# Kernel optimization log

Hardware: AMD Instinct MI355X
Metric: run time of the kernel (lower is better)

The kernel has to match this reference:

```python
import jax, jax.numpy as jnp
import numpy as np

N_NODES = 100000
EPS = 1e-12  # F.normalize eps


def _sage_conv(x, src, dst, deg, Wl, bl, Wr):
    # mean aggregation of neighbor (source) features at destination nodes
    agg = jax.ops.segment_sum(x[src], dst, num_segments=N_NODES)  # [N, F]
    agg = agg / jnp.maximum(deg, 1.0)[:, None]
    out = agg @ Wl + bl + x @ Wr  # lin_l(mean(x_j)) + lin_r(x_i)
    # normalize=True -> L2 row normalization
    norm = jnp.sqrt(jnp.sum(out * out, axis=-1, keepdims=True))
    return out / jnp.maximum(norm, EPS)


def setup_inputs() -> dict:
    key = jax.random.key(0)
    ks = jax.random.split(key, 10)
    F_IN, H, C = 14, 32, 2
    x = jax.random.normal(ks[0], (N_NODES, F_IN), dtype=jnp.float32)
    edge_index = jax.random.randint(ks[1], (2, 6400000), 0, N_NODES, dtype=jnp.int32)
    def glorot(k, shape):
        lim = float(np.sqrt(6.0 / (shape[0] + shape[1])))
        return jax.random.uniform(k, shape, jnp.float32, -lim, lim)
    return {
        "x": x,
        "edge_index": edge_index,
        "W1l": glorot(ks[2], (F_IN, H)), "b1": jnp.zeros((H,), jnp.float32),
        "W1r": glorot(ks[3], (F_IN, H)),
        "W2l": glorot(ks[4], (H, H)), "b2": jnp.zeros((H,), jnp.float32),
        "W2r": glorot(ks[5], (H, H)),
        "Wlin": glorot(ks[6], (H, C)), "blin": jnp.zeros((C,), jnp.float32),
    }


def reference(x, edge_index, W1l, b1, W1r, W2l, b2, W2r, Wlin, blin):
    src, dst = edge_index[0], edge_index[1]
    deg = jax.ops.segment_sum(jnp.ones_like(dst, dtype=x.dtype), dst,
                              num_segments=N_NODES)  # in-degree per node
    h = jax.nn.relu(_sage_conv(x, src, dst, deg, W1l, b1, W1r))
    # dropout p=0.2 is identity at inference
    h = jax.nn.relu(_sage_conv(h, src, dst, deg, W2l, b2, W2r))
    return h @ Wlin + blin  # [N, num_classes]
```

## Files before the change

kernel.cpp:

```cpp
#include <hip/hip_runtime.h>
#include <hip/hip_bf16.h>


#define CHA 16384
#define MAXBH 800
#define CAPH 9728

static __device__ __forceinline__ unsigned short f2bf(float f) {
    unsigned u = __float_as_uint(f);
    unsigned r = (u + 0x7FFFu + ((u >> 16) & 1u)) >> 16;
    return (unsigned short)r;
}
#define BF_LO(u) __uint_as_float((u) << 16)
#define BF_HI(u) __uint_as_float((u) & 0xFFFF0000u)

__global__ __launch_bounds__(1024) void partitionA(
        const float* __restrict__ x, unsigned short* __restrict__ xb,
        const int* __restrict__ src, const int* __restrict__ dst,
        int* __restrict__ bcursor, unsigned* __restrict__ part,
        int E, int N, int NBH) {
    __shared__ unsigned pk[CHA];
    __shared__ int h[MAXBH], lofs[MAXBH], delta[MAXBH];
    int t = threadIdx.x;
    int base = blockIdx.x * CHA;
    int end = base + CHA; if (end > E) end = E;
    int cnt = end - base;

    for (int i = blockIdx.x * 1024 + t; i < N * 16; i += gridDim.x * 1024) {
        int n = i >> 4, f = i & 15;
        float v = (f < 14) ? x[n * 14 + f] : 0.f;
        xb[i] = f2bf(v);
    }

    int ed[16], es[16], er[16];
    for (int i = t; i < NBH; i += 1024) h[i] = 0;
    __syncthreads();
    #pragma unroll
    for (int i = 0; i < 4; ++i) {
        int j = i * 4096 + t * 4;
        if (j + 4 <= cnt) {
            int4 d4 = *(const int4*)(dst + base + j);
            int4 s4 = *(const int4*)(src + base + j);
            ed[i*4+0] = d4.x; ed[i*4+1] = d4.y; ed[i*4+2] = d4.z; ed[i*4+3] = d4.w;
            es[i*4+0] = s4.x; es[i*4+1] = s4.y; es[i*4+2] = s4.z; es[i*4+3] = s4.w;
            er[i*4+0] = atomicAdd(&h[d4.x >> 7], 1);
            er[i*4+1] = atomicAdd(&h[d4.y >> 7], 1);
            er[i*4+2] = atomicAdd(&h[d4.z >> 7], 1);
            er[i*4+3] = atomicAdd(&h[d4.w >> 7], 1);
        } else {
            #pragma unroll
            for (int k = 0; k < 4; ++k) {
                if (j + k < cnt) {
                    ed[i*4+k] = dst[base + j + k];
                    es[i*4+k] = src[base + j + k];
                    er[i*4+k] = atomicAdd(&h[ed[i*4+k] >> 7], 1);
                } else ed[i*4+k] = -1;
            }
        }
    }
    __syncthreads();
    if (t < 64) {
        int vals[13];
        int run = 0;
        int b13 = t * 13;
        #pragma unroll
        for (int i = 0; i < 13; ++i) {
            int idx = b13 + i;
            int xv = (idx < NBH) ? h[idx] : 0;
            run += xv;
            vals[i] = run;
        }
        int tot = run, sc = run;
        #pragma unroll
        for (int off = 1; off < 64; off <<= 1) {
            int nv = __shfl_up(sc, off);
            if (t >= off) sc += nv;
        }
        int excl = sc - tot;
        #pragma unroll
        for (int i = 0; i < 13; ++i) {
            int idx = b13 + i;
            if (idx < NBH) {
                h[idx] = excl + vals[i];
                lofs[idx] = excl + (i ? vals[i - 1] : 0);
            }
        }
    }
    __syncthreads();
    if (t < NBH) {
        int excl = lofs[t];
        int v = h[t] - excl;
        int g = v ? atomicAdd(&bcursor[t], v) : 0;
        delta[t] = t * CAPH + g - excl;
    }
    __syncthreads();
    #pragma unroll
    for (int i = 0; i < 16; ++i) {
        int d = ed[i];
        if (d >= 0) {
            int b = d >> 7;
            pk[lofs[b] + er[i]] = ((unsigned)(d & 127) << 24) | (unsigned)es[i];
        }
    }
    __syncthreads();
    int wid = t >> 6, lane = t & 63;
    for (int b = wid; b < NBH; b += 16) {
        int s = lofs[b];
        int e2 = h[b];
        int dlt = delta[b];
        int lim = (b + 1) * CAPH;
        for (int k = s + lane; k < e2; k += 64) {
            int gidx = dlt + k;
            if (gidx < lim) part[gidx] = pk[k];
        }
    }
}

__global__ __launch_bounds__(1024) void partitionB_sort(
        const unsigned* __restrict__ part, const int* __restrict__ bcursor,
        int* __restrict__ deg, int* __restrict__ offs, int* __restrict__ nlo,
        int* __restrict__ sorted_src, int N, int HALF) {
    __shared__ int pk2[CAPH];
    __shared__ int hh[256], keyofs[256];
    __shared__ int sTot;
    int hbid = blockIdx.x;
    int t = threadIdx.x;
    int start = hbid * CAPH;
    int cc = bcursor[hbid];
    if (cc > CAPH) cc = CAPH;
    int end = start + cc;
    unsigned ce[10];
    int rk[10];
    if (t < 256) hh[t] = 0;
    __syncthreads();
    #pragma unroll
    for (int i = 0; i < 10; ++i) {
        int idx = start + t + i * 1024;
        unsigned p = 0xFFFFFFFFu;
        int r = 0;
        if (idx < end) {
            p = part[idx];
            int key = (int)(p >> 24) * 2 + (((int)(p & 0xFFFFFFu) < HALF) ? 0 : 1);
            r = atomicAdd(&hh[key], 1);
        }
        ce[i] = p;
        rk[i] = r;
    }
    __syncthreads();
    if (t < 64) {
        int b4 = t * 4;
        int v0 = hh[b4], v1 = hh[b4 + 1], v2 = hh[b4 + 2], v3 = hh[b4 + 3];
        int s1 = v0 + v1, s2 = s1 + v2, s3 = s2 + v3;
        int sc = s3;
        #pragma unroll
        for (int off = 1; off < 64; off <<= 1) {
            int nv = __shfl_up(sc, off);
            if (t >= off) sc += nv;
        }
        int excl = sc - s3;
        keyofs[b4]     = excl;
        keyofs[b4 + 1] = excl + v0;
        keyofs[b4 + 2] = excl + s1;
        keyofs[b4 + 3] = excl + s2;
        if (t == 63) sTot = excl + s3;
    }
    __syncthreads();
    if (t < 128) {
        int lo = hh[2 * t];
        int d = lo + hh[2 * t + 1];
        int excl = keyofs[2 * t];
        int node = hbid * 128 + t;
        if (node < N) {
            deg[node] = d;
            offs[node] = start + excl;
            nlo[node] = lo;
        }
    }
    #pragma unroll
    for (int i = 0; i < 10; ++i) {
        unsigned p = ce[i];
        if (p != 0xFFFFFFFFu) {
            int s = (int)(p & 0xFFFFFFu);
            int key = (int)(p >> 24) * 2 + ((s < HALF) ? 0 : 1);
            int pos = keyofs[key] + rk[i];
            if (pos < CAPH) pk2[pos] = s;
        }
    }
    __syncthreads();
    int tot = sTot; if (tot > CAPH) tot = CAPH;
    for (int i = t; i < tot; i += 1024)
        sorted_src[start + i] = pk2[i];
}

__global__ __launch_bounds__(256) void gather14_dense1(
        const uint4* __restrict__ xb4, const float* __restrict__ x,
        const int* __restrict__ sorted_src, const int* __restrict__ offs,
        const int* __restrict__ deg,
        const float* __restrict__ W1l, const float* __restrict__ b1,
        const float* __restrict__ W1r,
        float* __restrict__ hbuf, unsigned short* __restrict__ hb, int N) {
    __shared__ float swl[448], swr[448], sb1[32];
    int t = threadIdx.x;
    for (int i = t; i < 448; i += 256) { swl[i] = W1l[i]; swr[i] = W1r[i]; }
    if (t < 32) sb1[t] = b1[t];
    __syncthreads();

    int node = blockIdx.x * 32 + (t >> 3);
    int sub = t & 7, ep = sub >> 1, half = sub & 1;
    int lanebase = (t & 63) & ~7;
    bool valid = node < N;
    int js = valid ? offs[node] : 0;
    int d  = valid ? deg[node] : 0;
    int je = js + d;
    float x0 = 0.f, x1 = 0.f;
    if (valid && sub < 7) {
        x0 = x[node * 14 + sub * 2];
        x1 = x[node * 14 + sub * 2 + 1];
    }

    float a[8] = {0,0,0,0,0,0,0,0};
    int j = js + ep;
    for (; j + 12 < je; j += 16) {
        int s0 = sorted_src[j], s1 = sorted_src[j + 4];
        int s2 = sorted_src[j + 8], s3 = sorted_src[j + 12];
        uint4 u0 = xb4[s0 * 2 + half], u1 = xb4[s1 * 2 + half];
        uint4 u2 = xb4[s2 * 2 + half], u3 = xb4[s3 * 2 + half];
        a[0] += (BF_LO(u0.x) + BF_LO(u1.x)) + (BF_LO(u2.x) + BF_LO(u3.x));
        a[1] += (BF_HI(u0.x) + BF_HI(u1.x)) + (BF_HI(u2.x) + BF_HI(u3.x));
        a[2] += (BF_LO(u0.y) + BF_LO(u1.y)) + (BF_LO(u2.y) + BF_LO(u3.y));
        a[3] += (BF_HI(u0.y) + BF_HI(u1.y)) + (BF_HI(u2.y) + BF_HI(u3.y));
        a[4] += (BF_LO(u0.z) + BF_LO(u1.z)) + (BF_LO(u2.z) + BF_LO(u3.z));
        a[5] += (BF_HI(u0.z) + BF_HI(u1.z)) + (BF_HI(u2.z) + BF_HI(u3.z));
        a[6] += (BF_LO(u0.w) + BF_LO(u1.w)) + (BF_LO(u2.w) + BF_LO(u3.w));
        a[7] += (BF_HI(u0.w) + BF_HI(u1.w)) + (BF_HI(u2.w) + BF_HI(u3.w));
    }
    for (; j + 4 < je; j += 8) {
        int s0 = sorted_src[j], s1 = sorted_src[j + 4];
        uint4 u0 = xb4[s0 * 2 + half], u1 = xb4[s1 * 2 + half];
        a[0] += BF_LO(u0.x) + BF_LO(u1.x);
        a[1] += BF_HI(u0.x) + BF_HI(u1.x);
        a[2] += BF_LO(u0.y) + BF_LO(u1.y);
        a[3] += BF_HI(u0.y) + BF_HI(u1.y);
        a[4] += BF_LO(u0.z) + BF_LO(u1.z);
        a[5] += BF_HI(u0.z) + BF_HI(u1.z);
        a[6] += BF_LO(u0.w) + BF_LO(u1.w);
        a[7] += BF_HI(u0.w) + BF_HI(u1.w);
    }
    for (; j < je; j += 4) {
        uint4 u0 = xb4[sorted_src[j] * 2 + half];
        a[0] += BF_LO(u0.x); a[1] += BF_HI(u0.x);
        a[2] += BF_LO(u0.y); a[3] += BF_HI(u0.y);
        a[4] += BF_LO(u0.z); a[5] += BF_HI(u0.z);
        a[6] += BF_LO(u0.w); a[7] += BF_HI(u0.w);
    }
    #pragma unroll
    for (int i = 0; i < 8; ++i) {
        a[i] += __shfl_xor(a[i], 2);
        a[i] += __shfl_xor(a[i], 4);
    }

    float inv = 1.0f / ((d > 0) ? (float)d : 1.0f);
    float acc[4];
    #pragma unroll
    for (int i = 0; i < 4; ++i) acc[i] = sb1[sub * 4 + i];
    #pragma unroll
    for (int k = 0; k < 14; ++k) {
        float ag = __shfl(a[k & 7], lanebase + (k >> 3)) * inv;
        float xv = __shfl((k & 1) ? x1 : x0, lanebase + (k >> 1));
        float4 wl = *(const float4*)&swl[k * 32 + sub * 4];
        float4 wr = *(const float4*)&swr[k * 32 + sub * 4];
        acc[0] += ag * wl.x + xv * wr.x;
        acc[1] += ag * wl.y + xv * wr.y;
        acc[2] += ag * wl.z + xv * wr.z;
        acc[3] += ag * wl.w + xv * wr.w;
    }
    float ss = 0.f;
    #pragma unroll
    for (int i = 0; i < 4; ++i) ss += acc[i] * acc[i];
    ss += __shfl_xor(ss, 1); ss += __shfl_xor(ss, 2); ss += __shfl_xor(ss, 4);
    float invn = 1.f / fmaxf(sqrtf(ss), 1e-12f);
    if (valid) {
        float hv[4];
        #pragma unroll
        for (int i = 0; i < 4; ++i) hv[i] = fmaxf(acc[i] * invn, 0.f);
        *(float4*)(hbuf + (size_t)node * 32 + sub * 4) =
            make_float4(hv[0], hv[1], hv[2], hv[3]);
        uint2 pb;
        pb.x = (unsigned)f2bf(hv[0]) | ((unsigned)f2bf(hv[1]) << 16);
        pb.y = (unsigned)f2bf(hv[2]) | ((unsigned)f2bf(hv[3]) << 16);
        *(uint2*)(hb + (size_t)node * 32 + sub * 4) = pb;
    }
}

__global__ __launch_bounds__(256) void gather32_p0(
        const uint4* __restrict__ hb, const int* __restrict__ sorted_src,
        const int* __restrict__ offs, const int* __restrict__ nlo,
        float4* __restrict__ agg2a, int N) {
    int idx = blockIdx.x * blockDim.x + threadIdx.x;
    int n = idx >> 2;
    if (n >= N) return;
    int q = idx & 3;
    int start = offs[n];
    int jend = nlo[n];
    float a0=0,a1=0,a2=0,a3=0,a4=0,a5=0,a6=0,a7=0;
    int j = 0;
    for (; j + 8 <= jend; j += 8) {
        int s0 = sorted_src[start + j + 0];
        int s1 = sorted_src[start + j + 1];
        int s2 = sorted_src[start + j + 2];
        int s3 = sorted_src[start + j + 3];
        int s4 = sorted_src[start + j + 4];
        int s5 = sorted_src[start + j + 5];
        int s6 = sorted_src[start + j + 6];
        int s7 = sorted_src[start + j + 7];
        uint4 u0 = hb[s0 * 4 + q];
        uint4 u1 = hb[s1 * 4 + q];
        uint4 u2 = hb[s2 * 4 + q];
        uint4 u3 = hb[s3 * 4 + q];
        uint4 u4 = hb[s4 * 4 + q];
        uint4 u5 = hb[s5 * 4 + q];
        uint4 u6 = hb[s6 * 4 + q];
        uint4 u7 = hb[s7 * 4 + q];
        a0 += (BF_LO(u0.x)+BF_LO(u1.x)+BF_LO(u2.x)+BF_LO(u3.x))
            + (BF_LO(u4.x)+BF_LO(u5.x)+BF_LO(u6.x)+BF_LO(u7.x));
        a1 += (BF_HI(u0.x)+BF_HI(u1.x)+BF_HI(u2.x)+BF_HI(u3.x))
            + (BF_HI(u4.x)+BF_HI(u5.x)+BF_HI(u6.x)+BF_HI(u7.x));
        a2 += (BF_LO(u0.y)+BF_LO(u1.y)+BF_LO(u2.y)+BF_LO(u3.y))
            + (BF_LO(u4.y)+BF_LO(u5.y)+BF_LO(u6.y)+BF_LO(u7.y));
        a3 += (BF_HI(u0.y)+BF_HI(u1.y)+BF_HI(u2.y)+BF_HI(u3.y))
            + (BF_HI(u4.y)+BF_HI(u5.y)+BF_HI(u6.y)+BF_HI(u7.y));
        a4 += (BF_LO(u0.z)+BF_LO(u1.z)+BF_LO(u2.z)+BF_LO(u3.z))
            + (BF_LO(u4.z)+BF_LO(u5.z)+BF_LO(u6.z)+BF_LO(u7.z));
        a5 += (BF_HI(u0.z)+BF_HI(u1.z)+BF_HI(u2.z)+BF_HI(u3.z))
            + (BF_HI(u4.z)+BF_HI(u5.z)+BF_HI(u6.z)+BF_HI(u7.z));
        a6 += (BF_LO(u0.w)+BF_LO(u1.w)+BF_LO(u2.w)+BF_LO(u3.w))
            + (BF_LO(u4.w)+BF_LO(u5.w)+BF_LO(u6.w)+BF_LO(u7.w));
        a7 += (BF_HI(u0.w)+BF_HI(u1.w)+BF_HI(u2.w)+BF_HI(u3.w))
            + (BF_HI(u4.w)+BF_HI(u5.w)+BF_HI(u6.w)+BF_HI(u7.w));
    }
    for (; j + 4 <= jend; j += 4) {
        int s0 = sorted_src[start + j + 0];
        int s1 = sorted_src[start + j + 1];
        int s2 = sorted_src[start + j + 2];
        int s3 = sorted_src[start + j + 3];
        uint4 u0 = hb[s0 * 4 + q];
        uint4 u1 = hb[s1 * 4 + q];
        uint4 u2 = hb[s2 * 4 + q];
        uint4 u3 = hb[s3 * 4 + q];
        a0 += BF_LO(u0.x)+BF_LO(u1.x)+BF_LO(u2.x)+BF_LO(u3.x);
        a1 += BF_HI(u0.x)+BF_HI(u1.x)+BF_HI(u2.x)+BF_HI(u3.x);
        a2 += BF_LO(u0.y)+BF_LO(u1.y)+BF_LO(u2.y)+BF_LO(u3.y);
        a3 += BF_HI(u0.y)+BF_HI(u1.y)+BF_HI(u2.y)+BF_HI(u3.y);
        a4 += BF_LO(u0.z)+BF_LO(u1.z)+BF_LO(u2.z)+BF_LO(u3.z);
        a5 += BF_HI(u0.z)+BF_HI(u1.z)+BF_HI(u2.z)+BF_HI(u3.z);
        a6 += BF_LO(u0.w)+BF_LO(u1.w)+BF_LO(u2.w)+BF_LO(u3.w);
        a7 += BF_HI(u0.w)+BF_HI(u1.w)+BF_HI(u2.w)+BF_HI(u3.w);
    }
    for (; j < jend; ++j) {
        uint4 u0 = hb[sorted_src[start + j] * 4 + q];
        a0 += BF_LO(u0.x); a1 += BF_HI(u0.x);
        a2 += BF_LO(u0.y); a3 += BF_HI(u0.y);
        a4 += BF_LO(u0.z); a5 += BF_HI(u0.z);
        a6 += BF_LO(u0.w); a7 += BF_HI(u0.w);
    }
    agg2a[n * 8 + q * 2 + 0] = make_float4(a0, a1, a2, a3);
    agg2a[n * 8 + q * 2 + 1] = make_float4(a4, a5, a6, a7);
}

__global__ __launch_bounds__(256) void gather32p1_dense2(
        const uint4* __restrict__ hb, const int* __restrict__ sorted_src,
        const int* __restrict__ offs, const int* __restrict__ deg,
        const int* __restrict__ nlo, const float* __restrict__ agg2a,
        const float* __restrict__ hbuf,
        const float* __restrict__ W2l, const float* __restrict__ b2,
        const float* __restrict__ W2r, const float* __restrict__ Wlin,
        const float* __restrict__ blin, float* __restrict__ out, int N) {
    __shared__ float sa[64 * 33];
    __shared__ float sh2[64 * 33];
    __shared__ float swl[1024], swr[1024], swo[64], sb[32], sbo[2];
    int t = threadIdx.x;
    for (int i = t; i < 1024; i += 256) { swl[i] = W2l[i]; swr[i] = W2r[i]; }
    if (t < 64) swo[t] = Wlin[t];
    if (t < 32) sb[t] = b2[t];
    if (t < 2) sbo[t] = blin[t];

    int row = t >> 2, q = t & 3;
    int n = blockIdx.x * 64 + row;
    bool valid = n < N;
    int start = valid ? offs[n] : 0;
    int d = valid ? deg[n] : 0;
    int j = valid ? nlo[n] : 0;
    float a0=0,a1=0,a2=0,a3=0,a4=0,a5=0,a6=0,a7=0;
    for (; j + 8 <= d; j += 8) {
        int s0 = sorted_src[start + j + 0];
        int s1 = sorted_src[start + j + 1];
        int s2 = sorted_src[start + j + 2];
        int s3 = sorted_src[start + j + 3];
        int s4 = sorted_src[start + j + 4];
        int s5 = sorted_src[start + j + 5];
        int s6 = sorted_src[start + j + 6];
        int s7 = sorted_src[start + j + 7];
        uint4 u0 = hb[s0 * 4 + q];
        uint4 u1 = hb[s1 * 4 + q];
        uint4 u2 = hb[s2 * 4 + q];
        uint4 u3 = hb[s3 * 4 + q];
        uint4 u4 = hb[s4 * 4 + q];
        uint4 u5 = hb[s5 * 4 + q];
        uint4 u6 = hb[s6 * 4 + q];
        uint4 u7 = hb[s7 * 4 + q];
        a0 += (BF_LO(u0.x)+BF_LO(u1.x)+BF_LO(u2.x)+BF_LO(u3.x))
            + (BF_LO(u4.x)+BF_LO(u5.x)+BF_LO(u6.x)+BF_LO(u7.x));
        a1 += (BF_HI(u0.x)+BF_HI(u1.x)+BF_HI(u2.x)+BF_HI(u3.x))
            + (BF_HI(u4.x)+BF_HI(u5.x)+BF_HI(u6.x)+BF_HI(u7.x));
        a2 += (BF_LO(u0.y)+BF_LO(u1.y)+BF_LO(u2.y)+BF_LO(u3.y))
            + (BF_LO(u4.y)+BF_LO(u5.y)+BF_LO(u6.y)+BF_LO(u7.y));
        a3 += (BF_HI(u0.y)+BF_HI(u1.y)+BF_HI(u2.y)+BF_HI(u3.y))
            + (BF_HI(u4.y)+BF_HI(u5.y)+BF_HI(u6.y)+BF_HI(u7.y));
        a4 += (BF_LO(u0.z)+BF_LO(u1.z)+BF_LO(u2.z)+BF_LO(u3.z))
            + (BF_LO(u4.z)+BF_LO(u5.z)+BF_LO(u6.z)+BF_LO(u7.z));
        a5 += (BF_HI(u0.z)+BF_HI(u1.z)+BF_HI(u2.z)+BF_HI(u3.z))
            + (BF_HI(u4.z)+BF_HI(u5.z)+BF_HI(u6.z)+BF_HI(u7.z));
        a6 += (BF_LO(u0.w)+BF_LO(u1.w)+BF_LO(u2.w)+BF_LO(u3.w))
            + (BF_LO(u4.w)+BF_LO(u5.w)+BF_LO(u6.w)+BF_LO(u7.w));
        a7 += (BF_HI(u0.w)+BF_HI(u1.w)+BF_HI(u2.w)+BF_HI(u3.w))
            + (BF_HI(u4.w)+BF_HI(u5.w)+BF_HI(u6.w)+BF_HI(u7.w));
    }
    for (; j + 4 <= d; j += 4) {
        int s0 = sorted_src[start + j + 0];
        int s1 = sorted_src[start + j + 1];
        int s2 = sorted_src[start + j + 2];
        int s3 = sorted_src[start + j + 3];
        uint4 u0 = hb[s0 * 4 + q];
        uint4 u1 = hb[s1 * 4 + q];
        uint4 u2 = hb[s2 * 4 + q];
        uint4 u3 = hb[s3 * 4 + q];
        a0 += BF_LO(u0.x)+BF_LO(u1.x)+BF_LO(u2.x)+BF_LO(u3.x);
        a1 += BF_HI(u0.x)+BF_HI(u1.x)+BF_HI(u2.x)+BF_HI(u3.x);
        a2 += BF_LO(u0.y)+BF_LO(u1.y)+BF_LO(u2.y)+BF_LO(u3.y);
        a3 += BF_HI(u0.y)+BF_HI(u1.y)+BF_HI(u2.y)+BF_HI(u3.y);
        a4 += BF_LO(u0.z)+BF_LO(u1.z)+BF_LO(u2.z)+BF_LO(u3.z);
        a5 += BF_HI(u0.z)+BF_HI(u1.z)+BF_HI(u2.z)+BF_HI(u3.z);
        a6 += BF_LO(u0.w)+BF_LO(u1.w)+BF_LO(u2.w)+BF_LO(u3.w);
        a7 += BF_HI(u0.w)+BF_HI(u1.w)+BF_HI(u2.w)+BF_HI(u3.w);
    }
    for (; j < d; ++j) {
        uint4 u0 = hb[sorted_src[start + j] * 4 + q];
        a0 += BF_LO(u0.x); a1 += BF_HI(u0.x);
        a2 += BF_LO(u0.y); a3 += BF_HI(u0.y);
        a4 += BF_LO(u0.z); a5 += BF_HI(u0.z);
        a6 += BF_LO(u0.w); a7 += BF_HI(u0.w);
    }
    if (valid) {
        float inv = 1.0f / ((d > 0) ? (float)d : 1.0f);
        const float4* ga = (const float4*)(agg2a + (size_t)n * 32 + q * 8);
        float4 v0 = ga[0], v1 = ga[1];
        float* sd = &sa[row * 33 + q * 8];
        sd[0] = (v0.x + a0) * inv; sd[1] = (v0.y + a1) * inv;
        sd[2] = (v0.z + a2) * inv; sd[3] = (v0.w + a3) * inv;
        sd[4] = (v1.x + a4) * inv; sd[5] = (v1.y + a5) * inv;
        sd[6] = (v1.z + a6) * inv; sd[7] = (v1.w + a7) * inv;
        const float4* gh = (const float4*)(hbuf + (size_t)n * 32 + q * 8);
        float4 h0 = gh[0], h1 = gh[1];
        float* se = &sh2[row * 33 + q * 8];
        se[0] = h0.x; se[1] = h0.y; se[2] = h0.z; se[3] = h0.w;
        se[4] = h1.x; se[5] = h1.y; se[6] = h1.z; se[7] = h1.w;
    }
    __syncthreads();

    float acc[8];
    #pragma unroll
    for (int i = 0; i < 8; ++i) acc[i] = sb[q * 8 + i];
    for (int k = 0; k < 32; ++k) {
        float av = sa[row * 33 + k];
        float hv = sh2[row * 33 + k];
        const float4* wl4 = (const float4*)&swl[k * 32 + q * 8];
        const float4* wr4 = (const float4*)&swr[k * 32 + q * 8];
        float4 wla = wl4[0], wlb = wl4[1], wra = wr4[0], wrb = wr4[1];
        acc[0] += av * wla.x + hv * wra.x;
        acc[1] += av * wla.y + hv * wra.y;
        acc[2] += av * wla.z + hv * wra.z;
        acc[3] += av * wla.w + hv * wra.w;
        acc[4] += av * wlb.x + hv * wrb.x;
        acc[5] += av * wlb.y + hv * wrb.y;
        acc[6] += av * wlb.z + hv * wrb.z;
        acc[7] += av * wlb.w + hv * wrb.w;
    }
    float ss = 0.f;
    #pragma unroll
    for (int i = 0; i < 8; ++i) ss += acc[i] * acc[i];
    ss += __shfl_xor(ss, 1); ss += __shfl_xor(ss, 2);
    float invn = 1.f / fmaxf(sqrtf(ss), 1e-12f);
    float o0 = 0.f, o1 = 0.f;
    #pragma unroll
    for (int i = 0; i < 8; ++i) {
        float hv = fmaxf(acc[i] * invn, 0.f);
        int kk = q * 8 + i;
        o0 += hv * swo[kk * 2 + 0];
        o1 += hv * swo[kk * 2 + 1];
    }
    o0 += __shfl_xor(o0, 1); o0 += __shfl_xor(o0, 2);
    o1 += __shfl_xor(o1, 1); o1 += __shfl_xor(o1, 2);
    if (q == 0 && valid) {
        out[n * 2 + 0] = o0 + sbo[0];
        out[n * 2 + 1] = o1 + sbo[1];
    }
}

extern "C" void kernel_launch(void* const* d_in, const int* in_sizes, int n_in,
                              void* d_out, int out_size, void* d_ws, size_t ws_size,
                              hipStream_t stream) {
    const float* x    = (const float*)d_in[0];
    const int*   ei   = (const int*)d_in[1];
    const float* W1l  = (const float*)d_in[2];
    const float* b1   = (const float*)d_in[3];
    const float* W1r  = (const float*)d_in[4];
    const float* W2l  = (const float*)d_in[5];
    const float* b2   = (const float*)d_in[6];
    const float* W2r  = (const float*)d_in[7];
    const float* Wlin = (const float*)d_in[8];
    const float* blin = (const float*)d_in[9];
    float* out = (float*)d_out;

    const int N = in_sizes[0] / 14;
    const int E = in_sizes[1] / 2;
    const int* src = ei;
    const int* dst = ei + E;
    const int NBH = (N + 127) / 128;
    const int HALF = N / 2;

    char* ws = (char*)d_ws;
    size_t off = 0;
    auto alloc = [&](size_t bytes) -> void* {
        void* p = ws + off;
        off = (off + bytes + 255) & ~(size_t)255;
        return p;
    };
    int*            bcursor    = (int*)alloc((size_t)NBH * 4);
    unsigned*       part       = (unsigned*)alloc((size_t)NBH * CAPH * 4);
    int*            sorted_src = (int*)alloc((size_t)NBH * CAPH * 4);
    int*            deg        = (int*)alloc((size_t)N * 4);
    int*            offs       = (int*)alloc((size_t)N * 4);
    int*            nlo        = (int*)alloc((size_t)N * 4);
    unsigned short* xb         = (unsigned short*)alloc((size_t)N * 16 * 2);
    float*          hbuf       = (float*)alloc((size_t)N * 32 * 4);
    unsigned short* hb         = (unsigned short*)alloc((size_t)N * 32 * 2);
    float*          agg2a      = (float*)part;
    (void)ws_size; (void)n_in; (void)out_size;

    hipMemsetAsync(bcursor, 0, (size_t)NBH * 4, stream);
    partitionA<<<(E + CHA - 1) / CHA, 1024, 0, stream>>>(
        x, xb, src, dst, bcursor, part, E, N, NBH);
    partitionB_sort<<<NBH, 1024, 0, stream>>>(
        part, bcursor, deg, offs, nlo, sorted_src, N, HALF);
    gather14_dense1<<<(N + 31) / 32, 256, 0, stream>>>(
        (const uint4*)xb, x, sorted_src, offs, deg, W1l, b1, W1r, hbuf, hb, N);
    gather32_p0<<<(N * 4 + 255) / 256, 256, 0, stream>>>(
        (const uint4*)hb, sorted_src, offs, nlo, (float4*)agg2a, N);
    gather32p1_dense2<<<(N + 63) / 64, 256, 0, stream>>>(
        (const uint4*)hb, sorted_src, offs, deg, nlo, agg2a, hbuf,
        W2l, b2, W2r, Wlin, blin, out, N);
}
```

Baseline: 267.6 us.

## Fuse layer-1 gather into partition sort and merge split layer-2 gather

Folds the layer-1 neighbor gather and dense transform into the partition-sort kernel, so it reads source indices straight from shared memory instead of reloading sorted_src from global memory. Each block now covers 128 nodes with 1024 threads (8 per node). The two-pass layer-2 gather (low half, then high half through an agg2a buffer) becomes a single pass, which drops the nlo and agg2a traffic and one kernel launch. In exchange the split by source half, likely there for cache locality, is lost, and the fused kernel has a larger shared-memory footprint.

Measured after the change: 266.0 us. No clear change (-0.6%).

```diff
diff --git a/kernel.cpp b/kernel.cpp
--- a/kernel.cpp
+++ b/kernel.cpp
@@ -116,12 +116,18 @@
     }
 }
 
-__global__ __launch_bounds__(1024) void partitionB_sort(
+__global__ __launch_bounds__(1024) void partitionB_fused(
         const unsigned* __restrict__ part, const int* __restrict__ bcursor,
-        int* __restrict__ deg, int* __restrict__ offs, int* __restrict__ nlo,
-        int* __restrict__ sorted_src, int N, int HALF) {
+        const uint4* __restrict__ xb4, const float* __restrict__ x,
+        const float* __restrict__ W1l, const float* __restrict__ b1,
+        const float* __restrict__ W1r,
+        int* __restrict__ deg, int* __restrict__ offs,
+        int* __restrict__ sorted_src, float* __restrict__ hbuf,
+        unsigned short* __restrict__ hb, int N, int HALF) {
     __shared__ int pk2[CAPH];
     __shared__ int hh[256], keyofs[256];
+    __shared__ int lstart[128], ldeg[128];
+    __shared__ float swl[448], swr[448], sb1[32];
     __shared__ int sTot;
     int hbid = blockIdx.x;
     int t = threadIdx.x;
@@ -132,6 +138,8 @@
     unsigned ce[10];
     int rk[10];
     if (t < 256) hh[t] = 0;
+    if (t >= 512 && t < 960) { swl[t - 512] = W1l[t - 512]; swr[t - 512] = W1r[t - 512]; }
+    else if (t >= 960 && t < 992) sb1[t - 960] = b1[t - 960];
     __syncthreads();
     #pragma unroll
     for (int i = 0; i < 10; ++i) {
@@ -169,11 +177,12 @@
         int lo = hh[2 * t];
         int d = lo + hh[2 * t + 1];
         int excl = keyofs[2 * t];
+        lstart[t] = excl;
+        ldeg[t] = d;
         int node = hbid * 128 + t;
         if (node < N) {
             deg[node] = d;
             offs[node] = start + excl;
-            nlo[node] = lo;
         }
     }
     #pragma unroll
@@ -190,39 +199,23 @@
     int tot = sTot; if (tot > CAPH) tot = CAPH;
     for (int i = t; i < tot; i += 1024)
         sorted_src[start + i] = pk2[i];
-}
-
-__global__ __launch_bounds__(256) void gather14_dense1(
-        const uint4* __restrict__ xb4, const float* __restrict__ x,
-        const int* __restrict__ sorted_src, const int* __restrict__ offs,
-        const int* __restrict__ deg,
-        const float* __restrict__ W1l, const float* __restrict__ b1,
-        const float* __restrict__ W1r,
-        float* __restrict__ hbuf, unsigned short* __restrict__ hb, int N) {
-    __shared__ float swl[448], swr[448], sb1[32];
-    int t = threadIdx.x;
-    for (int i = t; i < 448; i += 256) { swl[i] = W1l[i]; swr[i] = W1r[i]; }
-    if (t < 32) sb1[t] = b1[t];
-    __syncthreads();
-
-    int node = blockIdx.x * 32 + (t >> 3);
-    int sub = t & 7, ep = sub >> 1, half = sub & 1;
+
+    int node = t >> 3, sub = t & 7, ep = sub >> 1, half = sub & 1;
     int lanebase = (t & 63) & ~7;
-    bool valid = node < N;
-    int js = valid ? offs[node] : 0;
-    int d  = valid ? deg[node] : 0;
+    int gnode = hbid * 128 + node;
+    bool valid = gnode < N;
+    int js = lstart[node], d = ldeg[node];
     int je = js + d;
     float x0 = 0.f, x1 = 0.f;
     if (valid && sub < 7) {
-        x0 = x[node * 14 + sub * 2];
-        x1 = x[node * 14 + sub * 2 + 1];
+        x0 = x[gnode * 14 + sub * 2];
+        x1 = x[gnode * 14 + sub * 2 + 1];
     }
 
     float a[8] = {0,0,0,0,0,0,0,0};
     int j = js + ep;
     for (; j + 12 < je; j += 16) {
-        int s0 = sorted_src[j], s1 = sorted_src[j + 4];
-        int s2 = sorted_src[j + 8], s3 = sorted_src[j + 12];
+        int s0 = pk2[j], s1 = pk2[j + 4], s2 = pk2[j + 8], s3 = pk2[j + 12];
         uint4 u0 = xb4[s0 * 2 + half], u1 = xb4[s1 * 2 + half];
         uint4 u2 = xb4[s2 * 2 + half], u3 = xb4[s3 * 2 + half];
         a[0] += (BF_LO(u0.x) + BF_LO(u1.x)) + (BF_LO(u2.x) + BF_LO(u3.x));
@@ -235,7 +228,7 @@
         a[7] += (BF_HI(u0.w) + BF_HI(u1.w)) + (BF_HI(u2.w) + BF_HI(u3.w));
     }
     for (; j + 4 < je; j += 8) {
-        int s0 = sorted_src[j], s1 = sorted_src[j + 4];
+        int s0 = pk2[j], s1 = pk2[j + 4];
         uint4 u0 = xb4[s0 * 2 + half], u1 = xb4[s1 * 2 + half];
         a[0] += BF_LO(u0.x) + BF_LO(u1.x);
         a[1] += BF_HI(u0.x) + BF_HI(u1.x);
@@ -247,7 +240,7 @@
         a[7] += BF_HI(u0.w) + BF_HI(u1.w);
     }
     for (; j < je; j += 4) {
-        uint4 u0 = xb4[sorted_src[j] * 2 + half];
+        uint4 u0 = xb4[pk2[j] * 2 + half];
         a[0] += BF_LO(u0.x); a[1] += BF_HI(u0.x);
         a[2] += BF_LO(u0.y); a[3] += BF_HI(u0.y);
         a[4] += BF_LO(u0.z); a[5] += BF_HI(u0.z);
@@ -283,94 +276,18 @@
         float hv[4];
         #pragma unroll
         for (int i = 0; i < 4; ++i) hv[i] = fmaxf(acc[i] * invn, 0.f);
-        *(float4*)(hbuf + (size_t)node * 32 + sub * 4) =
+        *(float4*)(hbuf + (size_t)gnode * 32 + sub * 4) =
             make_float4(hv[0], hv[1], hv[2], hv[3]);
         uint2 pb;
         pb.x = (unsigned)f2bf(hv[0]) | ((unsigned)f2bf(hv[1]) << 16);
         pb.y = (unsigned)f2bf(hv[2]) | ((unsigned)f2bf(hv[3]) << 16);
-        *(uint2*)(hb + (size_t)node * 32 + sub * 4) = pb;
+        *(uint2*)(hb + (size_t)gnode * 32 + sub * 4) = pb;
     }
 }
 
-__global__ __launch_bounds__(256) void gather32_p0(
-        const uint4* __restrict__ hb, const int* __restrict__ sorted_src,
-        const int* __restrict__ offs, const int* __restrict__ nlo,
-        float4* __restrict__ agg2a, int N) {
-    int idx = blockIdx.x * blockDim.x + threadIdx.x;
-    int n = idx >> 2;
-    if (n >= N) return;
-    int q = idx & 3;
-    int start = offs[n];
-    int jend = nlo[n];
-    float a0=0,a1=0,a2=0,a3=0,a4=0,a5=0,a6=0,a7=0;
-    int j = 0;
-    for (; j + 8 <= jend; j += 8) {
-        int s0 = sorted_src[start + j + 0];
-        int s1 = sorted_src[start + j + 1];
-        int s2 = sorted_src[start + j + 2];
-        int s3 = sorted_src[start + j + 3];
-        int s4 = sorted_src[start + j + 4];
-        int s5 = sorted_src[start + j + 5];
-        int s6 = sorted_src[start + j + 6];
-        int s7 = sorted_src[start + j + 7];
-        uint4 u0 = hb[s0 * 4 + q];
-        uint4 u1 = hb[s1 * 4 + q];
-        uint4 u2 = hb[s2 * 4 + q];
-        uint4 u3 = hb[s3 * 4 + q];
-        uint4 u4 = hb[s4 * 4 + q];
-        uint4 u5 = hb[s5 * 4 + q];
-        uint4 u6 = hb[s6 * 4 + q];
-        uint4 u7 = hb[s7 * 4 + q];
-        a0 += (BF_LO(u0.x)+BF_LO(u1.x)+BF_LO(u2.x)+BF_LO(u3.x))
-            + (BF_LO(u4.x)+BF_LO(u5.x)+BF_LO(u6.x)+BF_LO(u7.x));
-        a1 += (BF_HI(u0.x)+BF_HI(u1.x)+BF_HI(u2.x)+BF_HI(u3.x))
-            + (BF_HI(u4.x)+BF_HI(u5.x)+BF_HI(u6.x)+BF_HI(u7.x));
-        a2 += (BF_LO(u0.y)+BF_LO(u1.y)+BF_LO(u2.y)+BF_LO(u3.y))
-            + (BF_LO(u4.y)+BF_LO(u5.y)+BF_LO(u6.y)+BF_LO(u7.y));
-        a3 += (BF_HI(u0.y)+BF_HI(u1.y)+BF_HI(u2.y)+BF_HI(u3.y))
-            + (BF_HI(u4.y)+BF_HI(u5.y)+BF_HI(u6.y)+BF_HI(u7.y));
-        a4 += (BF_LO(u0.z)+BF_LO(u1.z)+BF_LO(u2.z)+BF_LO(u3.z))
-            + (BF_LO(u4.z)+BF_LO(u5.z)+BF_LO(u6.z)+BF_LO(u7.z));
-        a5 += (BF_HI(u0.z)+BF_HI(u1.z)+BF_HI(u2.z)+BF_HI(u3.z))
-            + (BF_HI(u4.z)+BF_HI(u5.z)+BF_HI(u6.z)+BF_HI(u7.z));
-        a6 += (BF_LO(u0.w)+BF_LO(u1.w)+BF_LO(u2.w)+BF_LO(u3.w))
-            + (BF_LO(u4.w)+BF_LO(u5.w)+BF_LO(u6.w)+BF_LO(u7.w));
-        a7 += (BF_HI(u0.w)+BF_HI(u1.w)+BF_HI(u2.w)+BF_HI(u3.w))
-            + (BF_HI(u4.w)+BF_HI(u5.w)+BF_HI(u6.w)+BF_HI(u7.w));
-    }
-    for (; j + 4 <= jend; j += 4) {
-        int s0 = sorted_src[start + j + 0];
-        int s1 = sorted_src[start + j + 1];
-        int s2 = sorted_src[start + j + 2];
-        int s3 = sorted_src[start + j + 3];
-        uint4 u0 = hb[s0 * 4 + q];
-        uint4 u1 = hb[s1 * 4 + q];
-        uint4 u2 = hb[s2 * 4 + q];
-        uint4 u3 = hb[s3 * 4 + q];
-        a0 += BF_LO(u0.x)+BF_LO(u1.x)+BF_LO(u2.x)+BF_LO(u3.x);
-        a1 += BF_HI(u0.x)+BF_HI(u1.x)+BF_HI(u2.x)+BF_HI(u3.x);
-        a2 += BF_LO(u0.y)+BF_LO(u1.y)+BF_LO(u2.y)+BF_LO(u3.y);
-        a3 += BF_HI(u0.y)+BF_HI(u1.y)+BF_HI(u2.y)+BF_HI(u3.y);
-        a4 += BF_LO(u0.z)+BF_LO(u1.z)+BF_LO(u2.z)+BF_LO(u3.z);
-        a5 += BF_HI(u0.z)+BF_HI(u1.z)+BF_HI(u2.z)+BF_HI(u3.z);
-        a6 += BF_LO(u0.w)+BF_LO(u1.w)+BF_LO(u2.w)+BF_LO(u3.w);
-        a7 += BF_HI(u0.w)+BF_HI(u1.w)+BF_HI(u2.w)+BF_HI(u3.w);
-    }
-    for (; j < jend; ++j) {
-        uint4 u0 = hb[sorted_src[start + j] * 4 + q];
-        a0 += BF_LO(u0.x); a1 += BF_HI(u0.x);
-        a2 += BF_LO(u0.y); a3 += BF_HI(u0.y);
-        a4 += BF_LO(u0.z); a5 += BF_HI(u0.z);
-        a6 += BF_LO(u0.w); a7 += BF_HI(u0.w);
-    }
-    agg2a[n * 8 + q * 2 + 0] = make_float4(a0, a1, a2, a3);
-    agg2a[n * 8 + q * 2 + 1] = make_float4(a4, a5, a6, a7);
-}
-
-__global__ __launch_bounds__(256) void gather32p1_dense2(
+__global__ __launch_bounds__(256) void gather32_dense2(
         const uint4* __restrict__ hb, const int* __restrict__ sorted_src,
         const int* __restrict__ offs, const int* __restrict__ deg,
-        const int* __restrict__ nlo, const float* __restrict__ agg2a,
         const float* __restrict__ hbuf,
         const float* __restrict__ W2l, const float* __restrict__ b2,
         const float* __restrict__ W2r, const float* __restrict__ Wlin,
@@ -389,8 +306,8 @@
     bool valid = n < N;
     int start = valid ? offs[n] : 0;
     int d = valid ? deg[n] : 0;
-    int j = valid ? nlo[n] : 0;
     float a0=0,a1=0,a2=0,a3=0,a4=0,a5=0,a6=0,a7=0;
+    int j = 0;
     for (; j + 8 <= d; j += 8) {
         int s0 = sorted_src[start + j + 0];
         int s1 = sorted_src[start + j + 1];
@@ -452,13 +369,9 @@
     }
     if (valid) {
         float inv = 1.0f / ((d > 0) ? (float)d : 1.0f);
-        const float4* ga = (const float4*)(agg2a + (size_t)n * 32 + q * 8);
-        float4 v0 = ga[0], v1 = ga[1];
         float* sd = &sa[row * 33 + q * 8];
-        sd[0] = (v0.x + a0) * inv; sd[1] = (v0.y + a1) * inv;
-        sd[2] = (v0.z + a2) * inv; sd[3] = (v0.w + a3) * inv;
-        sd[4] = (v1.x + a4) * inv; sd[5] = (v1.y + a5) * inv;
-        sd[6] = (v1.z + a6) * inv; sd[7] = (v1.w + a7) * inv;
+        sd[0] = a0 * inv; sd[1] = a1 * inv; sd[2] = a2 * inv; sd[3] = a3 * inv;
+        sd[4] = a4 * inv; sd[5] = a5 * inv; sd[6] = a6 * inv; sd[7] = a7 * inv;
         const float4* gh = (const float4*)(hbuf + (size_t)n * 32 + q * 8);
         float4 h0 = gh[0], h1 = gh[1];
         float* se = &sh2[row * 33 + q * 8];
@@ -540,23 +453,18 @@
     int*            sorted_src = (int*)alloc((size_t)NBH * CAPH * 4);
     int*            deg        = (int*)alloc((size_t)N * 4);
     int*            offs       = (int*)alloc((size_t)N * 4);
-    int*            nlo        = (int*)alloc((size_t)N * 4);
     unsigned short* xb         = (unsigned short*)alloc((size_t)N * 16 * 2);
     float*          hbuf       = (float*)alloc((size_t)N * 32 * 4);
     unsigned short* hb         = (unsigned short*)alloc((size_t)N * 32 * 2);
-    float*          agg2a      = (float*)part;
     (void)ws_size; (void)n_in; (void)out_size;
 
     hipMemsetAsync(bcursor, 0, (size_t)NBH * 4, stream);
     partitionA<<<(E + CHA - 1) / CHA, 1024, 0, stream>>>(
         x, xb, src, dst, bcursor, part, E, N, NBH);
-    partitionB_sort<<<NBH, 1024, 0, stream>>>(
-        part, bcursor, deg, offs, nlo, sorted_src, N, HALF);
-    gather14_dense1<<<(N + 31) / 32, 256, 0, stream>>>(
-        (const uint4*)xb, x, sorted_src, offs, deg, W1l, b1, W1r, hbuf, hb, N);
-    gather32_p0<<<(N * 4 + 255) / 256, 256, 0, stream>>>(
-        (const uint4*)hb, sorted_src, offs, nlo, (float4*)agg2a, N);
-    gather32p1_dense2<<<(N + 63) / 64, 256, 0, stream>>>(
-        (const uint4*)hb, sorted_src, offs, deg, nlo, agg2a, hbuf,
+    partitionB_fused<<<NBH, 1024, 0, stream>>>(
+        part, bcursor, (const uint4*)xb, x, W1l, b1, W1r,
+        deg, offs, sorted_src, hbuf, hb, N, HALF);
+    gather32_dense2<<<(N + 63) / 64, 256, 0, stream>>>(
+        (const uint4*)hb, sorted_src, offs, deg, hbuf,
         W2l, b2, W2r, Wlin, blin, out, N);
 }
```
